# Performance work log

Hardware: AMD Instinct MI355X
Metric: run time of the kernel (lower is better)

## Reference

```python
import jax, jax.numpy as jnp
import numpy as np

D_MODEL = 96
D_STATE = 1
D_CONV = 3
SSM_RATIO = 2.0
D_INNER = int(D_MODEL * SSM_RATIO)   # 192
DT_RANK = int(np.ceil(D_MODEL / 16))  # 6
K = 4                                 # scan directions
BSZ, H, W = 4, 128, 128


def setup_inputs() -> dict:
    key = jax.random.key(0)
    ks = jax.random.split(key, 8)
    x = jax.random.normal(ks[0], (BSZ, D_MODEL, H, W), jnp.float32)
    in_w = jax.random.normal(ks[1], (D_INNER, D_MODEL), jnp.float32) * (D_MODEL ** -0.5)
    in_b = jnp.zeros((D_INNER,), jnp.float32)
    dw_w = jax.random.normal(ks[2], (D_INNER, 1, D_CONV, D_CONV), jnp.float32) * (1.0 / D_CONV)
    dw_b = jnp.zeros((D_INNER,), jnp.float32)
    x_proj_weight = jax.random.normal(ks[3], (K, DT_RANK + 2 * D_STATE, D_INNER), jnp.float32) * 0.02
    dt_projs_weight = jax.random.normal(ks[4], (K, D_INNER, DT_RANK), jnp.float32) * (DT_RANK ** -0.5)
    # mamba dt init: bias = softplus^{-1}(dt), dt ~ U[dt_min, dt_max]
    dt = jax.random.uniform(ks[5], (K, D_INNER), jnp.float32, 0.001, 0.1)
    dt_projs_bias = jnp.log(jnp.expm1(dt))
    A_logs = jnp.zeros((K * D_INNER, D_STATE), jnp.float32)  # log(arange(1,N+1)), N=1 -> 0
    Ds = jnp.ones((K * D_INNER,), jnp.float32)
    ln_w = jnp.ones((D_INNER,), jnp.float32)
    ln_b = jnp.zeros((D_INNER,), jnp.float32)
    out_w = jax.random.normal(ks[6], (D_MODEL, D_INNER), jnp.float32) * (D_INNER ** -0.5)
    out_b = jnp.zeros((D_MODEL,), jnp.float32)
    return {"x": x, "in_w": in_w, "in_b": in_b, "dw_w": dw_w, "dw_b": dw_b,
            "x_proj_weight": x_proj_weight, "dt_projs_weight": dt_projs_weight,
            "dt_projs_bias": dt_projs_bias, "A_logs": A_logs, "Ds": Ds,
            "ln_w": ln_w, "ln_b": ln_b, "out_w": out_w, "out_b": out_b}


def _forward(x, in_w, in_b, dw_w, dw_b, x_proj_weight, dt_projs_weight,
             dt_projs_bias, A_logs, Ds, ln_w, ln_b, out_w, out_b):
    B = x.shape[0]
    L = H * W
    # ---- in_proj: 1x1 conv -> depthwise conv -> SiLU ----
    z = jnp.einsum('bchw,dc->bdhw', x, in_w) + in_b[None, :, None, None]
    z = jax.lax.conv_general_dilated(z, dw_w, (1, 1), 'SAME',
                                     feature_group_count=D_INNER,
                                     dimension_numbers=('NCHW', 'OIHW', 'NCHW'))
    z = z + dw_b[None, :, None, None]
    z = z * jax.nn.sigmoid(z)  # SiLU
    # ---- cross scan: 4 directions [B,K,D,L] ----
    x0 = z.reshape(B, D_INNER, L)                          # row-major
    x1 = jnp.swapaxes(z, 2, 3).reshape(B, D_INNER, L)      # column-major
    xs = jnp.stack([x0, x1, jnp.flip(x0, -1), jnp.flip(x1, -1)], axis=1)
    # ---- x_proj (grouped 1x1 conv over L) ----
    x_dbl = jnp.einsum('bkdl,ked->bkel', xs, x_proj_weight)  # e = R + 2N
    dts_r = x_dbl[:, :, :DT_RANK]                            # [B,K,R,L]
    Bs = x_dbl[:, :, DT_RANK:DT_RANK + D_STATE]              # [B,K,N,L]
    Cs = x_dbl[:, :, DT_RANK + D_STATE:]                     # [B,K,N,L]
    dts = jnp.einsum('bkrl,kdr->bkdl', dts_r, dt_projs_weight)
    # ---- selective scan (fp32, delta_softplus=True) ----
    delta = jax.nn.softplus(dts + dt_projs_bias[None, :, :, None])     # [B,K,D,L]
    A = -jnp.exp(A_logs.astype(jnp.float32)).reshape(K, D_INNER, D_STATE)
    dA = jnp.exp(delta[..., None] * A[None, :, :, None, :])            # [B,K,D,L,N]
    Bt = jnp.swapaxes(Bs, 2, 3)                                        # [B,K,L,N]
    dBu = delta[..., None] * Bt[:, :, None] * xs[..., None]            # [B,K,D,L,N]

    def combine(c1, c2):
        a1, b1 = c1
        a2, b2 = c2
        return a1 * a2, b1 * a2 + b2

    _, hs = jax.lax.associative_scan(combine, (dA, dBu), axis=3)       # h_t states
    Ct = jnp.swapaxes(Cs, 2, 3)                                        # [B,K,L,N]
    y = jnp.einsum('bkdln,bkln->bkdl', hs, Ct) \
        + Ds.reshape(K, D_INNER)[None, :, :, None] * xs
    # ---- cross merge (inverse of cross scan, summed) ----
    y0 = y[:, 0]
    y1 = jnp.swapaxes(y[:, 1].reshape(B, D_INNER, W, H), 2, 3).reshape(B, D_INNER, L)
    y2 = jnp.flip(y[:, 2], -1)
    y3 = jnp.swapaxes(jnp.flip(y[:, 3], -1).reshape(B, D_INNER, W, H), 2, 3).reshape(B, D_INNER, L)
    ym = (y0 + y1 + y2 + y3).reshape(B, D_INNER, H, W).astype(x.dtype)
    # ---- out_proj: LayerNorm2d (over channels) + 1x1 conv ----
    yn = jnp.moveaxis(ym, 1, -1)  # [B,H,W,C]
    mu = yn.mean(-1, keepdims=True)
    var = yn.var(-1, keepdims=True)
    yn = (yn - mu) * jax.lax.rsqrt(var + 1e-5) * ln_w + ln_b
    yn = jnp.moveaxis(yn, -1, 1)
    return jnp.einsum('bdhw,cd->bchw', yn, out_w) + out_b[None, :, None, None]


def reference(x, in_w, in_b, dw_w, dw_b, x_proj_weight, dt_projs_weight,
              dt_projs_bias, A_logs, Ds, ln_w, ln_b, out_w, out_b):
    return _forward(x, in_w, in_b, dw_w, dw_b, x_proj_weight, dt_projs_weight,
                    dt_projs_bias, A_logs, Ds, ln_w, ln_b, out_w, out_b)
```

## Files before the change

kernel.cpp:

```cpp
#include <hip/hip_runtime.h>
#include <math.h>

#define D_MODEL 96
#define D_INNER 192
#define DT_RANK 6
#define K4      4
#define BSZ     4
#define HH      128
#define WW      128
#define LL      16384

#define LOG2E 1.4426950408889634f
#define LN2   0.6931471805599453f

#if __has_builtin(__builtin_amdgcn_exp2f)
__device__ __forceinline__ float fexp2_(float x){ return __builtin_amdgcn_exp2f(x); }
#else
__device__ __forceinline__ float fexp2_(float x){ return exp2f(x); }
#endif
#if __has_builtin(__builtin_amdgcn_logf)
__device__ __forceinline__ float flog2_(float x){ return __builtin_amdgcn_logf(x); }
#else
__device__ __forceinline__ float flog2_(float x){ return log2f(x); }
#endif
#if __has_builtin(__builtin_amdgcn_rcpf)
__device__ __forceinline__ float frcp_(float x){ return __builtin_amdgcn_rcpf(x); }
#else
__device__ __forceinline__ float frcp_(float x){ return 1.0f/x; }
#endif

__device__ __forceinline__ float softplus_fast(float x){
    return fmaxf(x, 0.0f) + LN2 * flog2_(1.0f + fexp2_(-LOG2E * fabsf(x)));
}
__device__ __forceinline__ float silu_fast(float x){
    return x * frcp_(1.0f + fexp2_(-LOG2E * x));
}

__global__ __launch_bounds__(512) void k_inproj(const float* __restrict__ x,
                                                const float* __restrict__ in_w,
                                                const float* __restrict__ in_b,
                                                float* __restrict__ z0) {
    const int blk = blockIdx.x;
    const int b  = blk >> 8;
    const int l0 = (blk & 255) << 6;
    const int p = threadIdx.x & 63;
    const int g = __builtin_amdgcn_readfirstlane(threadIdx.x >> 6);
    const float* xb = x + (size_t)b * D_MODEL * LL + l0 + p;
    float* zb = z0 + (size_t)b * D_INNER * LL + l0 + p;
    for (int jb = 0; jb < 3; ++jb) {
        const int d0 = g * 24 + jb * 8;
        float acc[8];
        #pragma unroll
        for (int j = 0; j < 8; ++j) acc[j] = in_b[d0 + j];
        const float* w0 = in_w + (size_t)d0 * D_MODEL;
        #pragma unroll 4
        for (int c = 0; c < D_MODEL; ++c) {
            float v = xb[(size_t)c * LL];
            #pragma unroll
            for (int j = 0; j < 8; ++j)
                acc[j] = fmaf(w0[c + j * D_MODEL], v, acc[j]);
        }
        #pragma unroll
        for (int j = 0; j < 8; ++j) zb[(size_t)(d0 + j) * LL] = acc[j];
    }
}

__global__ __launch_bounds__(256) void k_dwconv(const float* __restrict__ z0,
                                                const float* __restrict__ dw_w,
                                                const float* __restrict__ dw_b,
                                                float* __restrict__ z,
                                                float* __restrict__ zT) {
    __shared__ float tin[34][34];
    __shared__ float tout[32][33];
    const int blk  = blockIdx.x;
    const int tile = blk & 15;
    const int bd   = blk >> 4;
    const int d    = bd % D_INNER;
    const int h0 = (tile >> 2) << 5, w0 = (tile & 3) << 5;
    const float* src = z0 + (size_t)bd * LL;
    for (int i = threadIdx.x; i < 34 * 34; i += 256) {
        int r = i / 34, c = i - r * 34;
        int hh = h0 + r - 1, ww = w0 + c - 1;
        float v = 0.0f;
        if (hh >= 0 && hh < HH && ww >= 0 && ww < WW) v = src[hh * WW + ww];
        tin[r][c] = v;
    }
    __syncthreads();
    float wreg[9];
    #pragma unroll
    for (int i = 0; i < 9; ++i) wreg[i] = dw_w[d * 9 + i];
    const float bias = dw_b[d];
    #pragma unroll
    for (int i = 0; i < 4; ++i) {
        int idx = threadIdx.x + i * 256;
        int r = idx >> 5, c = idx & 31;
        float acc = bias;
        #pragma unroll
        for (int ky = 0; ky < 3; ++ky)
            #pragma unroll
            for (int kx = 0; kx < 3; ++kx)
                acc = fmaf(wreg[ky * 3 + kx], tin[r + ky][c + kx], acc);
        acc = silu_fast(acc);
        tout[r][c] = acc;
        z[(size_t)bd * LL + (h0 + r) * WW + w0 + c] = acc;
    }
    __syncthreads();
    #pragma unroll
    for (int i = 0; i < 4; ++i) {
        int idx = threadIdx.x + i * 256;
        int r = idx >> 5, c = idx & 31;
        zT[(size_t)bd * LL + (w0 + r) * HH + h0 + c] = tout[c][r];
    }
}

__global__ __launch_bounds__(256) void k_proj(const float* __restrict__ z,
                                              const float* __restrict__ zT,
                                              const float* __restrict__ xpw,
                                              float* __restrict__ dtsr,
                                              float* __restrict__ Bs,
                                              float* __restrict__ Cs) {
    const int blk = blockIdx.x;
    const int seg = blk >> 10;
    const int rest = blk & 1023;
    const int b  = rest >> 8;
    const int l0 = (rest & 255) << 6;
    const int kA = seg ? 1 : 0;
    const int kB = seg ? 3 : 2;
    const float* src = seg ? zT : z;
    const int p = threadIdx.x & 63;
    const int g = __builtin_amdgcn_readfirstlane(threadIdx.x >> 6);
    const float* sb = src + (size_t)b * D_INNER * LL + l0 + p;
    const int k  = (g < 2) ? kA : kB;
    const int e0 = (g & 1) * 4;
    const float* wrow = xpw + (size_t)(k * 8 + e0) * D_INNER;
    float a0 = 0.f, a1 = 0.f, a2 = 0.f, a3 = 0.f;
    #pragma unroll 8
    for (int dd = 0; dd < D_INNER; ++dd) {
        float v = sb[(size_t)dd * LL];
        a0 = fmaf(wrow[dd],               v, a0);
        a1 = fmaf(wrow[dd + D_INNER],     v, a1);
        a2 = fmaf(wrow[dd + 2 * D_INNER], v, a2);
        a3 = fmaf(wrow[dd + 3 * D_INNER], v, a3);
    }
    const int l = l0 + p;
    const size_t dbase = ((size_t)(b * K4 + k) * DT_RANK) * LL;
    if (e0 == 0) {
        dtsr[dbase + 0 * LL + l] = a0;
        dtsr[dbase + 1 * LL + l] = a1;
        dtsr[dbase + 2 * LL + l] = a2;
        dtsr[dbase + 3 * LL + l] = a3;
    } else {
        dtsr[dbase + 4 * LL + l] = a0;
        dtsr[dbase + 5 * LL + l] = a1;
        Bs[(size_t)(b * K4 + k) * LL + l] = a2;
        Cs[(size_t)(b * K4 + k) * LL + l] = a3;
    }
}

template <bool FWD, bool RMW, bool LDSU>
__device__ __forceinline__ void scan_core(const float* __restrict__ u_lin,
                                          const float* __restrict__ u_rm,
                                          const float* __restrict__ dtsr_k,
                                          const float* __restrict__ B_k,
                                          const float* __restrict__ C_k,
                                          const float* __restrict__ w6p,
                                          float dtbv, float A2, float Dval,
                                          float* __restrict__ dst,
                                          float* __restrict__ wPs,
                                          float* __restrict__ wSs,
                                          float* __restrict__ tile) {
    const int tid  = threadIdx.x;
    const int lane = tid & 63;
    const int wv   = tid >> 6;
    float w6[6];
    #pragma unroll
    for (int r = 0; r < 6; ++r) w6[r] = w6p[r];
    float h0 = 0.0f;
    float4 pu0, pu1, pB0, pB1, pC0, pC1;
    if (!LDSU) {
        const int c0 = FWD ? 0 : 7;
        const int q0 = (c0 << 11) + (tid << 3);
        pu0 = *(const float4*)(u_lin + q0);
        pu1 = *(const float4*)(u_lin + q0 + 4);
        pB0 = *(const float4*)(B_k + q0);
        pB1 = *(const float4*)(B_k + q0 + 4);
        pC0 = *(const float4*)(C_k + q0);
        pC1 = *(const float4*)(C_k + q0 + 4);
    }
    for (int ci = 0; ci < 8; ++ci) {
        const int c  = FWD ? ci : (7 - ci);
        const int l0 = (c << 11) + (tid << 3);
        float u[8], Bv[8], Cv[8];
        if (LDSU) {
            #pragma unroll
            for (int e = 0; e < 8; ++e) {
                int idx = tid + (e << 8);
                int h = idx >> 4, w = idx & 15;
                tile[w * 132 + h] = u_rm[h * WW + (c << 4) + w];
            }
            __syncthreads();
            const int wl = tid >> 4;
            const int hb = (tid & 15) << 3;
            #pragma unroll
            for (int e = 0; e < 8; ++e) u[e] = tile[wl * 132 + hb + e];
            float4 t0 = *(const float4*)(B_k + l0);
            float4 t1 = *(const float4*)(B_k + l0 + 4);
            Bv[0]=t0.x; Bv[1]=t0.y; Bv[2]=t0.z; Bv[3]=t0.w;
            Bv[4]=t1.x; Bv[5]=t1.y; Bv[6]=t1.z; Bv[7]=t1.w;
            t0 = *(const float4*)(C_k + l0);
            t1 = *(const float4*)(C_k + l0 + 4);
            Cv[0]=t0.x; Cv[1]=t0.y; Cv[2]=t0.z; Cv[3]=t0.w;
            Cv[4]=t1.x; Cv[5]=t1.y; Cv[6]=t1.z; Cv[7]=t1.w;
        } else {
            u[0]=pu0.x; u[1]=pu0.y; u[2]=pu0.z; u[3]=pu0.w;
            u[4]=pu1.x; u[5]=pu1.y; u[6]=pu1.z; u[7]=pu1.w;
            Bv[0]=pB0.x; Bv[1]=pB0.y; Bv[2]=pB0.z; Bv[3]=pB0.w;
            Bv[4]=pB1.x; Bv[5]=pB1.y; Bv[6]=pB1.z; Bv[7]=pB1.w;
            Cv[0]=pC0.x; Cv[1]=pC0.y; Cv[2]=pC0.z; Cv[3]=pC0.w;
            Cv[4]=pC1.x; Cv[5]=pC1.y; Cv[6]=pC1.z; Cv[7]=pC1.w;
            if (ci < 7) {
                const int cn = FWD ? (ci + 1) : (6 - ci);
                const int qn = (cn << 11) + (tid << 3);
                pu0 = *(const float4*)(u_lin + qn);
                pu1 = *(const float4*)(u_lin + qn + 4);
                pB0 = *(const float4*)(B_k + qn);
                pB1 = *(const float4*)(B_k + qn + 4);
                pC0 = *(const float4*)(C_k + qn);
                pC1 = *(const float4*)(C_k + qn + 4);
            }
        }
        float dl[8];
        #pragma unroll
        for (int e = 0; e < 8; ++e) dl[e] = dtbv;
        #pragma unroll
        for (int r = 0; r < 6; ++r) {
            float4 t0 = *(const float4*)(dtsr_k + (size_t)r * LL + l0);
            float4 t1 = *(const float4*)(dtsr_k + (size_t)r * LL + l0 + 4);
            dl[0] = fmaf(w6[r], t0.x, dl[0]); dl[1] = fmaf(w6[r], t0.y, dl[1]);
            dl[2] = fmaf(w6[r], t0.z, dl[2]); dl[3] = fmaf(w6[r], t0.w, dl[3]);
            dl[4] = fmaf(w6[r], t1.x, dl[4]); dl[5] = fmaf(w6[r], t1.y, dl[5]);
            dl[6] = fmaf(w6[r], t1.z, dl[6]); dl[7] = fmaf(w6[r], t1.w, dl[7]);
        }
        float a[8], bb[8];
        #pragma unroll
        for (int e = 0; e < 8; ++e) {
            float d1 = softplus_fast(dl[e]);
            a[e]  = fexp2_(d1 * A2);
            bb[e] = d1 * Bv[e] * u[e];
        }
        float P = 1.0f, S = 0.0f;
        if (FWD) {
            #pragma unroll
            for (int e = 0; e < 8; ++e) { S = fmaf(S, a[e], bb[e]); P *= a[e]; }
        } else {
            #pragma unroll
            for (int e = 7; e >= 0; --e) { S = fmaf(S, a[e], bb[e]); P *= a[e]; }
        }
        #pragma unroll
        for (int s = 1; s < 64; s <<= 1) {
            float p2, s2;
            if (FWD) { p2 = __shfl_up(P, s);   s2 = __shfl_up(S, s); }
            else     { p2 = __shfl_down(P, s); s2 = __shfl_down(S, s); }
            const bool act = FWD ? (lane >= s) : (lane + s < 64);
            if (act) { S = fmaf(s2, P, S); P = p2 * P; }
        }
        __syncthreads();
        if ((FWD && lane == 63) || (!FWD && lane == 0)) { wPs[wv] = P; wSs[wv] = S; }
        __syncthreads();
        float Pw = 1.0f, Sw = 0.0f;
        if (FWD) { for (int w2 = 0; w2 < wv; ++w2)  { Sw = fmaf(Sw, wPs[w2], wSs[w2]); Pw *= wPs[w2]; } }
        else     { for (int w2 = 3; w2 > wv; --w2)  { Sw = fmaf(Sw, wPs[w2], wSs[w2]); Pw *= wPs[w2]; } }
        float Pex, Sex;
        if (FWD) { Pex = __shfl_up(P, 1);   Sex = __shfl_up(S, 1);   if (lane == 0)  { Pex = 1.0f; Sex = 0.0f; } }
        else     { Pex = __shfl_down(P, 1); Sex = __shfl_down(S, 1); if (lane == 63) { Pex = 1.0f; Sex = 0.0f; } }
        float h = fmaf(Pw, h0, Sw);
        h = fmaf(Pex, h, Sex);
        float Pt = 1.0f, St = 0.0f;
        if (FWD) { for (int w2 = 0; w2 < 4; ++w2)  { St = fmaf(St, wPs[w2], wSs[w2]); Pt *= wPs[w2]; } }
        else     { for (int w2 = 3; w2 >= 0; --w2) { St = fmaf(St, wPs[w2], wSs[w2]); Pt *= wPs[w2]; } }
        h0 = fmaf(Pt, h0, St);
        float y[8];
        if (FWD) {
            #pragma unroll
            for (int e = 0; e < 8; ++e) { h = fmaf(a[e], h, bb[e]); y[e] = fmaf(h, Cv[e], Dval * u[e]); }
        } else {
            #pragma unroll
            for (int e = 7; e >= 0; --e) { h = fmaf(a[e], h, bb[e]); y[e] = fmaf(h, Cv[e], Dval * u[e]); }
        }
        if (!RMW) {
            *(float4*)(dst + l0)     = make_float4(y[0], y[1], y[2], y[3]);
            *(float4*)(dst + l0 + 4) = make_float4(y[4], y[5], y[6], y[7]);
        } else {
            float4 o0 = *(const float4*)(dst + l0);
            float4 o1 = *(const float4*)(dst + l0 + 4);
            o0.x += y[0]; o0.y += y[1]; o0.z += y[2]; o0.w += y[3];
            o1.x += y[4]; o1.y += y[5]; o1.z += y[6]; o1.w += y[7];
            *(float4*)(dst + l0)     = o0;
            *(float4*)(dst + l0 + 4) = o1;
        }
    }
}

__global__ __launch_bounds__(256) void k_scanA(const float* __restrict__ z,
                                               float* __restrict__ zT,
                                               float* __restrict__ y_r,
                                               const float* __restrict__ dtsr,
                                               const float* __restrict__ Bs,
                                               const float* __restrict__ Cs,
                                               const float* __restrict__ dtw,
                                               const float* __restrict__ dtb,
                                               const float* __restrict__ A_logs,
                                               const float* __restrict__ Ds) {
    __shared__ float wPs[4], wSs[4];
    const int blk = blockIdx.x;
    const int half = blk >= 768;
    const int bd = half ? blk - 768 : blk;
    const int b = bd / D_INNER, d = bd - b * D_INNER;
    const int k = half ? 3 : 0;
    const int kd = k * D_INNER + d;
    const float* dk = dtsr + ((size_t)(b * K4 + k) * DT_RANK) * LL;
    const float* Bk = Bs + (size_t)(b * K4 + k) * LL;
    const float* Ck = Cs + (size_t)(b * K4 + k) * LL;
    const float* w6p = dtw + (size_t)kd * 6;
    const float A2 = -expf(A_logs[kd]) * LOG2E;
    if (!half)
        scan_core<true, false, false>(z + (size_t)bd * LL, nullptr, dk, Bk, Ck, w6p,
                                      dtb[kd], A2, Ds[kd], y_r + (size_t)bd * LL,
                                      wPs, wSs, nullptr);
    else
        scan_core<false, false, false>(zT + (size_t)bd * LL, nullptr, dk, Bk, Ck, w6p,
                                       dtb[kd], A2, Ds[kd], zT + (size_t)bd * LL,
                                       wPs, wSs, nullptr);
}

__global__ __launch_bounds__(256) void k_scanB(const float* __restrict__ z,
                                               float* __restrict__ zT,
                                               float* __restrict__ y_r,
                                               const float* __restrict__ dtsr,
                                               const float* __restrict__ Bs,
                                               const float* __restrict__ Cs,
                                               const float* __restrict__ dtw,
                                               const float* __restrict__ dtb,
                                               const float* __restrict__ A_logs,
                                               const float* __restrict__ Ds) {
    __shared__ float wPs[4], wSs[4];
    __shared__ float tile[16 * 132];
    const int blk = blockIdx.x;
    const int half = blk >= 768;
    const int bd = half ? blk - 768 : blk;
    const int b = bd / D_INNER, d = bd - b * D_INNER;
    const int k = half ? 1 : 2;
    const int kd = k * D_INNER + d;
    const float* dk = dtsr + ((size_t)(b * K4 + k) * DT_RANK) * LL;
    const float* Bk = Bs + (size_t)(b * K4 + k) * LL;
    const float* Ck = Cs + (size_t)(b * K4 + k) * LL;
    const float* w6p = dtw + (size_t)kd * 6;
    const float A2 = -expf(A_logs[kd]) * LOG2E;
    if (!half)
        scan_core<false, true, false>(z + (size_t)bd * LL, nullptr, dk, Bk, Ck, w6p,
                                      dtb[kd], A2, Ds[kd], y_r + (size_t)bd * LL,
                                      wPs, wSs, nullptr);
    else
        scan_core<true, true, true>(nullptr, z + (size_t)bd * LL, dk, Bk, Ck, w6p,
                                    dtb[kd], A2, Ds[kd], zT + (size_t)bd * LL,
                                    wPs, wSs, tile);
}

__global__ __launch_bounds__(256) void k_taddT(const float* __restrict__ ym2,
                                               float* __restrict__ ym) {
    __shared__ float t[32][33];
    const int blk  = blockIdx.x;
    const int tile = blk & 15;
    const int bd   = blk >> 4;
    const int h0 = (tile >> 2) << 5, w0 = (tile & 3) << 5;
    const float* s = ym2 + (size_t)bd * LL;
    float* o = ym + (size_t)bd * LL;
    for (int i = threadIdx.x; i < 1024; i += 256) {
        int r = i >> 5, c = i & 31;
        t[r][c] = s[(w0 + r) * HH + h0 + c];
    }
    __syncthreads();
    for (int i = threadIdx.x; i < 1024; i += 256) {
        int r = i >> 5, c = i & 31;
        o[(h0 + r) * WW + w0 + c] += t[c][r];
    }
}

__global__ __launch_bounds__(512) void k_lnout(const float* __restrict__ ym,
                                               const float* __restrict__ ln_w,
                                               const float* __restrict__ ln_b,
                                               const float* __restrict__ out_w,
                                               const float* __restrict__ out_b,
                                               float* __restrict__ out) {
    __shared__ float red1[8][64];
    __shared__ float red2[8][64];
    const int blk = blockIdx.x;
    const int b  = blk >> 8;
    const int l0 = (blk & 255) << 6;
    const int p = threadIdx.x & 63;
    const int g = __builtin_amdgcn_readfirstlane(threadIdx.x >> 6);
    const float* vm = ym + (size_t)b * D_INNER * LL + l0 + p;
    float s1 = 0.f, s2 = 0.f;
    #pragma unroll 8
    for (int j = 0; j < 24; ++j) {
        float v = vm[(size_t)(g * 24 + j) * LL];
        s1 += v;
        s2 = fmaf(v, v, s2);
    }
    red1[g][p] = s1;
    red2[g][p] = s2;
    __syncthreads();
    float t1 = 0.f, t2 = 0.f;
    #pragma unroll
    for (int j = 0; j < 8; ++j) { t1 += red1[j][p]; t2 += red2[j][p]; }
    const float mu = t1 * (1.0f / 192.0f);
    const float rs = rsqrtf(t2 * (1.0f / 192.0f) - mu * mu + 1e-5f);
    float acc[12];
    #pragma unroll
    for (int cb = 0; cb < 12; ++cb) acc[cb] = 0.f;
    const float* wq = out_w + (size_t)g * 12 * D_INNER;
    #pragma unroll 8
    for (int dd = 0; dd < D_INNER; ++dd) {
        float v = vm[(size_t)dd * LL];
        float yn = fmaf((v - mu) * rs, ln_w[dd], ln_b[dd]);
        #pragma unroll
        for (int cb = 0; cb < 12; ++cb)
            acc[cb] = fmaf(wq[(size_t)cb * D_INNER + dd], yn, acc[cb]);
    }
    float* ob = out + (size_t)b * D_MODEL * LL + l0 + p;
    #pragma unroll
    for (int cb = 0; cb < 12; ++cb) {
        int cc = g * 12 + cb;
        ob[(size_t)cc * LL] = acc[cb] + out_b[cc];
    }
}

extern "C" void kernel_launch(void* const* d_in, const int* in_sizes, int n_in,
                              void* d_out, int out_size, void* d_ws, size_t ws_size,
                              hipStream_t stream) {
    (void)in_sizes; (void)n_in; (void)out_size; (void)ws_size;
    const float* x      = (const float*)d_in[0];
    const float* in_w   = (const float*)d_in[1];
    const float* in_b   = (const float*)d_in[2];
    const float* dw_w   = (const float*)d_in[3];
    const float* dw_b   = (const float*)d_in[4];
    const float* xpw    = (const float*)d_in[5];
    const float* dtw    = (const float*)d_in[6];
    const float* dtb    = (const float*)d_in[7];
    const float* A_logs = (const float*)d_in[8];
    const float* Ds     = (const float*)d_in[9];
    const float* ln_w   = (const float*)d_in[10];
    const float* ln_b   = (const float*)d_in[11];
    const float* out_w  = (const float*)d_in[12];
    const float* out_b  = (const float*)d_in[13];
    float* out = (float*)d_out;

    float* ws = (float*)d_ws;
    const size_t A1 = (size_t)BSZ * D_INNER * LL;
    float* z0   = ws;
    float* z    = ws + A1;
    float* zT   = ws + 2 * A1;
    float* dtsr = ws + 3 * A1;
    float* BsP  = dtsr + (size_t)BSZ * K4 * DT_RANK * LL;
    float* CsP  = BsP + (size_t)BSZ * K4 * LL;

    float* y_r = z0;

    k_inproj<<<1024, 512, 0, stream>>>(x, in_w, in_b, z0);
    k_dwconv<<<BSZ * D_INNER * 16, 256, 0, stream>>>(z0, dw_w, dw_b, z, zT);
    k_proj<<<2048, 256, 0, stream>>>(z, zT, xpw, dtsr, BsP, CsP);
    k_scanA<<<1536, 256, 0, stream>>>(z, zT, y_r, dtsr, BsP, CsP, dtw, dtb, A_logs, Ds);
    k_scanB<<<1536, 256, 0, stream>>>(z, zT, y_r, dtsr, BsP, CsP, dtw, dtb, A_logs, Ds);
    k_taddT<<<BSZ * D_INNER * 16, 256, 0, stream>>>(zT, y_r);
    k_lnout<<<1024, 512, 0, stream>>>(y_r, ln_w, ln_b, out_w, out_b, out);
}
```

Baseline: 397.7 us.

## Fuse transpose-add into LayerNorm/out-proj and fold LN affine into weights

Removes the separate transpose-add kernel: the final kernel reads the row-major and column-major scan outputs directly over 8x8 spatial tiles and sums them. LayerNorm is folded algebraically into the output projection through a small precompute kernel that builds weight*ln_w and per-channel sums. Statistics and the matmul then come from a single pass over the channels, with no second read and no shared-memory reduction. The cost is a less coalesced strided read of the column-major input, a slightly different numerical path (mean subtracted after the matmul), and one extra tiny kernel launch.

```diff
diff --git a/kernel.cpp b/kernel.cpp
--- a/kernel.cpp
+++ b/kernel.cpp
@@ -34,6 +34,35 @@
 }
 __device__ __forceinline__ float silu_fast(float x){
     return x * frcp_(1.0f + fexp2_(-LOG2E * x));
+}
+
+__global__ __launch_bounds__(64) void k_foldw(const float* __restrict__ out_w,
+                                              const float* __restrict__ ln_w,
+                                              const float* __restrict__ ln_b,
+                                              const float* __restrict__ out_b,
+                                              float* __restrict__ W2,
+                                              float* __restrict__ SS) {
+    const int c = blockIdx.x;
+    const int t = threadIdx.x;
+    float s1 = 0.f, s2 = 0.f;
+    #pragma unroll
+    for (int j = 0; j < 3; ++j) {
+        int d = t + j * 64;
+        float w  = out_w[c * D_INNER + d];
+        float w2 = w * ln_w[d];
+        W2[c * D_INNER + d] = w2;
+        s1 += w2;
+        s2 = fmaf(w, ln_b[d], s2);
+    }
+    #pragma unroll
+    for (int s = 32; s > 0; s >>= 1) {
+        s1 += __shfl_down(s1, s);
+        s2 += __shfl_down(s2, s);
+    }
+    if (t == 0) {
+        SS[c] = s1;
+        SS[96 + c] = s2 + out_b[c];
+    }
 }
 
 __global__ __launch_bounds__(512) void k_inproj(const float* __restrict__ x,
@@ -366,72 +395,41 @@
                                     wPs, wSs, tile);
 }
 
-__global__ __launch_bounds__(256) void k_taddT(const float* __restrict__ ym2,
-                                               float* __restrict__ ym) {
-    __shared__ float t[32][33];
-    const int blk  = blockIdx.x;
-    const int tile = blk & 15;
-    const int bd   = blk >> 4;
-    const int h0 = (tile >> 2) << 5, w0 = (tile & 3) << 5;
-    const float* s = ym2 + (size_t)bd * LL;
-    float* o = ym + (size_t)bd * LL;
-    for (int i = threadIdx.x; i < 1024; i += 256) {
-        int r = i >> 5, c = i & 31;
-        t[r][c] = s[(w0 + r) * HH + h0 + c];
-    }
-    __syncthreads();
-    for (int i = threadIdx.x; i < 1024; i += 256) {
-        int r = i >> 5, c = i & 31;
-        o[(h0 + r) * WW + w0 + c] += t[c][r];
-    }
-}
-
-__global__ __launch_bounds__(512) void k_lnout(const float* __restrict__ ym,
-                                               const float* __restrict__ ln_w,
-                                               const float* __restrict__ ln_b,
-                                               const float* __restrict__ out_w,
-                                               const float* __restrict__ out_b,
-                                               float* __restrict__ out) {
-    __shared__ float red1[8][64];
-    __shared__ float red2[8][64];
+__global__ __launch_bounds__(512) void k_lnout2(const float* __restrict__ y_r,
+                                                const float* __restrict__ y_c,
+                                                const float* __restrict__ W2,
+                                                const float* __restrict__ SS,
+                                                float* __restrict__ out) {
     const int blk = blockIdx.x;
     const int b  = blk >> 8;
-    const int l0 = (blk & 255) << 6;
+    const int t  = blk & 255;
+    const int h0 = (t >> 4) << 3, w0 = (t & 15) << 3;
     const int p = threadIdx.x & 63;
     const int g = __builtin_amdgcn_readfirstlane(threadIdx.x >> 6);
-    const float* vm = ym + (size_t)b * D_INNER * LL + l0 + p;
+    const int hr = p >> 3, wc = p & 7;
+    const float* ar = y_r + (size_t)b * D_INNER * LL + (h0 + hr) * WW + w0 + wc;
+    const float* ac = y_c + (size_t)b * D_INNER * LL + (w0 + wc) * HH + h0 + hr;
+    const float* wq = W2 + (size_t)g * 12 * D_INNER;
+    float acc[12];
+    #pragma unroll
+    for (int cb = 0; cb < 12; ++cb) acc[cb] = 0.f;
     float s1 = 0.f, s2 = 0.f;
-    #pragma unroll 8
-    for (int j = 0; j < 24; ++j) {
-        float v = vm[(size_t)(g * 24 + j) * LL];
+    #pragma unroll 4
+    for (int dd = 0; dd < D_INNER; ++dd) {
+        float v = ar[(size_t)dd * LL] + ac[(size_t)dd * LL];
         s1 += v;
         s2 = fmaf(v, v, s2);
-    }
-    red1[g][p] = s1;
-    red2[g][p] = s2;
-    __syncthreads();
-    float t1 = 0.f, t2 = 0.f;
-    #pragma unroll
-    for (int j = 0; j < 8; ++j) { t1 += red1[j][p]; t2 += red2[j][p]; }
-    const float mu = t1 * (1.0f / 192.0f);
-    const float rs = rsqrtf(t2 * (1.0f / 192.0f) - mu * mu + 1e-5f);
-    float acc[12];
-    #pragma unroll
-    for (int cb = 0; cb < 12; ++cb) acc[cb] = 0.f;
-    const float* wq = out_w + (size_t)g * 12 * D_INNER;
-    #pragma unroll 8
-    for (int dd = 0; dd < D_INNER; ++dd) {
-        float v = vm[(size_t)dd * LL];
-        float yn = fmaf((v - mu) * rs, ln_w[dd], ln_b[dd]);
         #pragma unroll
         for (int cb = 0; cb < 12; ++cb)
-            acc[cb] = fmaf(wq[(size_t)cb * D_INNER + dd], yn, acc[cb]);
-    }
-    float* ob = out + (size_t)b * D_MODEL * LL + l0 + p;
+            acc[cb] = fmaf(wq[cb * D_INNER + dd], v, acc[cb]);
+    }
+    const float mu = s1 * (1.0f / 192.0f);
+    const float rs = rsqrtf(s2 * (1.0f / 192.0f) - mu * mu + 1e-5f);
+    float* ob = out + (size_t)b * D_MODEL * LL + (h0 + hr) * WW + w0 + wc;
     #pragma unroll
     for (int cb = 0; cb < 12; ++cb) {
         int cc = g * 12 + cb;
-        ob[(size_t)cc * LL] = acc[cb] + out_b[cc];
+        ob[(size_t)cc * LL] = rs * (acc[cb] - mu * SS[cc]) + SS[96 + cc];
     }
 }
 
@@ -463,14 +461,16 @@
     float* dtsr = ws + 3 * A1;
     float* BsP  = dtsr + (size_t)BSZ * K4 * DT_RANK * LL;
     float* CsP  = BsP + (size_t)BSZ * K4 * LL;
+    float* W2   = CsP + (size_t)BSZ * K4 * LL;
+    float* SS   = W2 + (size_t)D_MODEL * D_INNER;
 
     float* y_r = z0;
 
+    k_foldw<<<96, 64, 0, stream>>>(out_w, ln_w, ln_b, out_b, W2, SS);
     k_inproj<<<1024, 512, 0, stream>>>(x, in_w, in_b, z0);
     k_dwconv<<<BSZ * D_INNER * 16, 256, 0, stream>>>(z0, dw_w, dw_b, z, zT);
     k_proj<<<2048, 256, 0, stream>>>(z, zT, xpw, dtsr, BsP, CsP);
     k_scanA<<<1536, 256, 0, stream>>>(z, zT, y_r, dtsr, BsP, CsP, dtw, dtb, A_logs, Ds);
     k_scanB<<<1536, 256, 0, stream>>>(z, zT, y_r, dtsr, BsP, CsP, dtw, dtb, A_logs, Ds);
-    k_taddT<<<BSZ * D_INNER * 16, 256, 0, stream>>>(zT, y_r);
-    k_lnout<<<1024, 512, 0, stream>>>(y_r, ln_w, ln_b, out_w, out_b, out);
-}
+    k_lnout2<<<1024, 512, 0, stream>>>(y_r, zT, W2, SS, out);
+}
```

Measured after the change: 442.2 us. 11.2% more time.
